# Kernel optimization log

Measured on AMD Instinct MI355X. Metric: run time of the kernel, lower is better.

Reference implementation:

```python
import jax, jax.numpy as jnp
import numpy as np

N, D, V = 4096, 512, 50000
K = 10  # accuracy_slack_size


def setup_inputs() -> dict:
    key = jax.random.key(0)
    k1, k2, k3, k4 = jax.random.split(key, 4)
    logits = jax.random.normal(k1, (N, D), dtype=jnp.float32)
    target = jax.random.randint(k2, (N,), 0, V, dtype=jnp.int64)
    mask = jax.random.randint(k3, (N,), 0, 2, dtype=jnp.int32)
    word_vectors = jax.random.normal(k4, (V, D), dtype=jnp.float32)
    return {"logits": logits, "target": target, "mask": mask, "word_vectors": word_vectors}


def reference(logits, target, mask, word_vectors):
    # Brute-force euclidean kNN: squared distances suffice for neighbor ranking.
    # d2[n, v] = ||x_n||^2 - 2 x_n . w_v + ||w_v||^2   -> [N, V]
    x2 = jnp.sum(logits * logits, axis=-1, keepdims=True)          # [N, 1]
    w2 = jnp.sum(word_vectors * word_vectors, axis=-1)             # [V]
    d2 = x2 - 2.0 * (logits @ word_vectors.T) + w2[None, :]        # [N, V]
    # top-K smallest distances -> indices of K nearest words
    _, words = jax.lax.top_k(-d2, K)                               # [N, K]
    # membership check: is the target word among the K neighbors
    hit = jnp.any(words == target[:, None], axis=-1)               # [N] bool
    m = mask.astype(jnp.float32)
    acc = jnp.sum(m * hit.astype(jnp.float32)) / jnp.sum(m)
    return jnp.reshape(acc, (1,))
```

## Files before the change

kernel.cpp:

```cpp
#include <hip/hip_runtime.h>
#include <stdint.h>

#define N_ROWS 4096
#define DIM    512
#define VOCAB  50000
#define VPAD   50048
#define TOPK   10
#define MARGIN 8.0f

typedef int i32x4 __attribute__((ext_vector_type(4)));

#define GLOBAL_AS __attribute__((address_space(1)))
#define LDS_AS    __attribute__((address_space(3)))

__device__ __forceinline__ void quant_row(const float* __restrict__ src,
                                          signed char* __restrict__ dst,
                                          int lane, float* rowmax_out,
                                          float* w2_out) {
    const float4* s4 = (const float4*)(src + lane * 8);
    float4 a = s4[0], b = s4[1];
    float mx = fmaxf(fmaxf(fmaxf(fabsf(a.x), fabsf(a.y)), fmaxf(fabsf(a.z), fabsf(a.w))),
                     fmaxf(fmaxf(fabsf(b.x), fabsf(b.y)), fmaxf(fabsf(b.z), fabsf(b.w))));
    float w2 = a.x*a.x + a.y*a.y + a.z*a.z + a.w*a.w
             + b.x*b.x + b.y*b.y + b.z*b.z + b.w*b.w;
    #pragma unroll
    for (int off = 1; off < 64; off <<= 1) {
        mx  = fmaxf(mx, __shfl_xor(mx, off, 64));
        w2 += __shfl_xor(w2, off, 64);
    }
    float inv = 127.0f / fmaxf(mx, 1e-30f);
    int q0 = (int)rintf(a.x * inv), q1 = (int)rintf(a.y * inv);
    int q2 = (int)rintf(a.z * inv), q3 = (int)rintf(a.w * inv);
    int q4 = (int)rintf(b.x * inv), q5 = (int)rintf(b.y * inv);
    int q6 = (int)rintf(b.z * inv), q7 = (int)rintf(b.w * inv);
    uint2 pk;
    pk.x = (q0 & 0xff) | ((q1 & 0xff) << 8) | ((q2 & 0xff) << 16) | ((unsigned)(q3 & 0xff) << 24);
    pk.y = (q4 & 0xff) | ((q5 & 0xff) << 8) | ((q6 & 0xff) << 16) | ((unsigned)(q7 & 0xff) << 24);
    *(uint2*)(dst + lane * 8) = pk;
    *rowmax_out = mx;
    *w2_out = w2;
}

#define PREP_Z  64
#define PREP_QX (PREP_Z + N_ROWS / 4)
#define PREP_QW (PREP_QX + VPAD / 4)
#define PREP_ST (PREP_QW + N_ROWS / 4)

__global__ __launch_bounds__(256) void prep_kernel(
        const float* __restrict__ X, const float* __restrict__ W,
        const int* __restrict__ target,
        signed char* __restrict__ Xq, signed char* __restrict__ Wq,
        float* __restrict__ sx, float* __restrict__ sw,
        float* __restrict__ w2, float* __restrict__ st,
        int* __restrict__ zbase) {
    const int b = blockIdx.x;
    const int wave = threadIdx.x >> 6, lane = threadIdx.x & 63;
    if (b < PREP_Z) {
        int i = b * 256 + threadIdx.x;
        if (i < 3 * N_ROWS + 16) zbase[i] = 0;
    } else if (b < PREP_QX) {
        int row = (b - PREP_Z) * 4 + wave;
        float mx, w2v;
        quant_row(X + (size_t)row * DIM, Xq + (size_t)row * DIM, lane, &mx, &w2v);
        if (lane == 0) sx[row] = fmaxf(mx, 1e-30f) / 127.0f;
    } else if (b < PREP_QW) {
        int row = (b - PREP_QX) * 4 + wave;
        if (row < VOCAB) {
            float mx, s2;
            quant_row(W + (size_t)row * DIM, Wq + (size_t)row * DIM, lane, &mx, &s2);
            if (lane == 0) { sw[row] = fmaxf(mx, 1e-30f) / 127.0f; w2[row] = s2; }
        } else {
            *(uint2*)(Wq + (size_t)row * DIM + lane * 8) = make_uint2(0, 0);
            if (lane == 0) { sw[row] = 0.0f; w2[row] = 1e30f; }
        }
    } else {
        int n = (b - PREP_QW) * 4 + wave;
        int t = target[n];
        const float4* x4 = (const float4*)(X + (size_t)n * DIM);
        const float4* w4 = (const float4*)(W + (size_t)t * DIM);
        float4 xa = x4[lane], xb = x4[lane + 64];
        float4 wa = w4[lane], wb = w4[lane + 64];
        float sxw = xa.x*wa.x + xa.y*wa.y + xa.z*wa.z + xa.w*wa.w
                  + xb.x*wb.x + xb.y*wb.y + xb.z*wb.z + xb.w*wb.w;
        float sww = wa.x*wa.x + wa.y*wa.y + wa.z*wa.z + wa.w*wa.w
                  + wb.x*wb.x + wb.y*wb.y + wb.z*wb.z + wb.w*wb.w;
        #pragma unroll
        for (int off = 32; off > 0; off >>= 1) {
            sxw += __shfl_down(sxw, off, 64);
            sww += __shfl_down(sww, off, 64);
        }
        if (lane == 0) st[n] = sww - 2.0f * sxw;
    }
}

__global__ __launch_bounds__(256) void count_mfma_i8(
        const signed char* __restrict__ Xq, const signed char* __restrict__ Wq,
        const float* __restrict__ sx, const float* __restrict__ sw,
        const float* __restrict__ w2, const float* __restrict__ st,
        const int* __restrict__ target,
        int* __restrict__ cnt_def, int* __restrict__ cnt_unc) {

    __shared__ signed char Als[128 * 64];
    __shared__ signed char Bls[128 * 64];
    __shared__ float w2_s[128];
    __shared__ float sw_s[128];
    __shared__ float st_s[128];
    __shared__ float sx_s[128];
    __shared__ int   t_s[128];
    __shared__ int   pk_s[128];

    const int tid  = threadIdx.x;
    const int wave = tid >> 6, lane = tid & 63;
    const int row0 = blockIdx.x * 128;
    const int col0 = blockIdx.y * 128;

    if (tid < 128) { w2_s[tid] = w2[col0 + tid]; sw_s[tid] = sw[col0 + tid]; pk_s[tid] = 0; }
    else           { st_s[tid - 128] = st[row0 + tid - 128];
                     sx_s[tid - 128] = sx[row0 + tid - 128];
                     t_s[tid - 128]  = target[row0 + tid - 128]; }

    const int ch = (lane & 3) ^ ((lane >> 3) & 3);
    const signed char* ga = Xq + (size_t)(row0 + wave*32 + (lane >> 2)) * DIM + ch * 16;
    const signed char* gb = Wq + (size_t)(col0 + wave*32 + (lane >> 2)) * DIM + ch * 16;
    signed char* la0 = &Als[(wave*32     ) * 64];
    signed char* la1 = &Als[(wave*32 + 16) * 64];
    signed char* lb0 = &Bls[(wave*32     ) * 64];
    signed char* lb1 = &Bls[(wave*32 + 16) * 64];

    const int q = lane >> 4, c = lane & 15;
    const int fs = (c >> 1) & 3;
    const int wm = wave >> 1, wn = wave & 1;
    const signed char* ap = &Als[(wm*64 + c) * 64 + (q ^ fs) * 16];
    const signed char* bp = &Bls[(wn*64 + c) * 64 + (q ^ fs) * 16];

    i32x4 acc[4][4];
    #pragma unroll
    for (int i = 0; i < 4; i++)
        #pragma unroll
        for (int j = 0; j < 4; j++) acc[i][j] = (i32x4){0, 0, 0, 0};

    for (int k0 = 0; k0 < DIM; k0 += 64) {
        __builtin_amdgcn_global_load_lds((const GLOBAL_AS void*)(ga + k0),           (LDS_AS void*)la0, 16, 0, 0);
        __builtin_amdgcn_global_load_lds((const GLOBAL_AS void*)(ga + 16*DIM + k0),  (LDS_AS void*)la1, 16, 0, 0);
        __builtin_amdgcn_global_load_lds((const GLOBAL_AS void*)(gb + k0),           (LDS_AS void*)lb0, 16, 0, 0);
        __builtin_amdgcn_global_load_lds((const GLOBAL_AS void*)(gb + 16*DIM + k0),  (LDS_AS void*)lb1, 16, 0, 0);
        __syncthreads();
        i32x4 af[4], bfr[4];
        #pragma unroll
        for (int i = 0; i < 4; i++) af[i]  = *(const i32x4*)(ap + i * 16 * 64);
        #pragma unroll
        for (int j = 0; j < 4; j++) bfr[j] = *(const i32x4*)(bp + j * 16 * 64);
        #pragma unroll
        for (int i = 0; i < 4; i++)
            #pragma unroll
            for (int j = 0; j < 4; j++)
                acc[i][j] = __builtin_amdgcn_mfma_i32_16x16x64_i8(af[i], bfr[j], acc[i][j], 0, 0, 0);
        __syncthreads();
    }

    #pragma unroll
    for (int i = 0; i < 4; i++) {
        #pragma unroll
        for (int reg = 0; reg < 4; reg++) {
            int r = wm*64 + i*16 + q*4 + reg;
            float stv = st_s[r];
            float sxr = sx_s[r];
            int   t   = t_s[r];
            int def = 0, unc = 0;
            #pragma unroll
            for (int j = 0; j < 4; j++) {
                int col_l = wn*64 + j*16 + c;
                float dot = sxr * sw_s[col_l] * (float)acc[i][j][reg];
                float s = w2_s[col_l] - 2.0f * dot;
                int v = col0 + col_l;
                if (v != t) {
                    if      (s < stv - MARGIN) def++;
                    else if (s < stv + MARGIN) unc++;
                }
            }
            int pk = (def << 16) | unc;
            pk += __shfl_xor(pk, 1, 64);
            pk += __shfl_xor(pk, 2, 64);
            pk += __shfl_xor(pk, 4, 64);
            pk += __shfl_xor(pk, 8, 64);
            if (c == 0) atomicAdd(&pk_s[r], pk);
        }
    }
    __syncthreads();
    if (tid < 128) {
        int pk = pk_s[tid];
        if (pk) {
            atomicAdd(&cnt_def[row0 + tid], pk >> 16);
            atomicAdd(&cnt_unc[row0 + tid], pk & 0xffff);
        }
    }
}

__global__ __launch_bounds__(256) void resolve3(const int* __restrict__ cnt_def,
                                                const int* __restrict__ cnt_unc,
                                                int* __restrict__ amb_rows,
                                                int* __restrict__ amb_count) {
    int n = blockIdx.x * 256 + threadIdx.x;
    if (n >= N_ROWS) return;
    int d = cnt_def[n], u = cnt_unc[n];
    if (d < TOPK && d + u >= TOPK) {
        int idx = atomicAdd(amb_count, 1);
        amb_rows[idx] = n;
    }
}

__device__ __forceinline__ int dot4i8(int a, int b, int acc) {
#if __has_builtin(__builtin_amdgcn_sdot4)
    return __builtin_amdgcn_sdot4(a, b, acc, false);
#else
    #pragma unroll
    for (int j = 0; j < 4; j++)
        acc += (int)(signed char)(a >> (8*j)) * (int)(signed char)(b >> (8*j));
    return acc;
#endif
}

__global__ __launch_bounds__(256) void band_scan(
        const signed char* __restrict__ Xq, const signed char* __restrict__ Wq,
        const float* __restrict__ X, const float* __restrict__ W,
        const float* __restrict__ sx, const float* __restrict__ sw,
        const float* __restrict__ w2, const float* __restrict__ st,
        const int* __restrict__ target,
        const int* __restrict__ amb_rows, const int* __restrict__ amb_count,
        int* __restrict__ count_exact) {
    const int lane = threadIdx.x & 63;
    const int wid  = (blockIdx.x << 2) | (threadIdx.x >> 6);
    const int nw   = gridDim.x << 2;
    const int namb = amb_count[0];
    for (int a = 0; a < namb; a++) {
        const int row = amb_rows[a];
        const int t   = target[row];
        const float sxr = sx[row], stv = st[row];
        const int2 xa8 = *(const int2*)(Xq + (size_t)row * DIM + lane * 8);
        for (int v = wid; v < VPAD; v += nw) {
            int2 wa8 = *(const int2*)(Wq + (size_t)v * DIM + lane * 8);
            int acc = dot4i8(xa8.x, wa8.x, 0);
            acc = dot4i8(xa8.y, wa8.y, acc);
            acc += __shfl_xor(acc, 1, 64);
            acc += __shfl_xor(acc, 2, 64);
            acc += __shfl_xor(acc, 4, 64);
            acc += __shfl_xor(acc, 8, 64);
            acc += __shfl_xor(acc, 16, 64);
            acc += __shfl_xor(acc, 32, 64);
            if (v == t) continue;
            float dot = sxr * sw[v] * (float)acc;
            float s = w2[v] - 2.0f * dot;
            if (!(s < stv - MARGIN) && (s < stv + MARGIN)) {
                const float4* xr = (const float4*)(X + (size_t)row * DIM + lane * 8);
                const float4* wr = (const float4*)(W + (size_t)v   * DIM + lane * 8);
                float4 x0 = xr[0], x1 = xr[1];
                float4 w0 = wr[0], w1 = wr[1];
                float p = x0.x*w0.x + x0.y*w0.y + x0.z*w0.z + x0.w*w0.w
                        + x1.x*w1.x + x1.y*w1.y + x1.z*w1.z + x1.w*w1.w;
                p += __shfl_xor(p, 1, 64);
                p += __shfl_xor(p, 2, 64);
                p += __shfl_xor(p, 4, 64);
                p += __shfl_xor(p, 8, 64);
                p += __shfl_xor(p, 16, 64);
                p += __shfl_xor(p, 32, 64);
                if (lane == 0) {
                    float se = w2[v] - 2.0f * p;
                    if (se < stv || (se == stv && v < t)) atomicAdd(&count_exact[row], 1);
                }
            }
        }
    }
}

__global__ __launch_bounds__(256) void finalize3(const int* __restrict__ cnt_def,
                                                 const int* __restrict__ cnt_unc,
                                                 const int* __restrict__ count_exact,
                                                 const int* __restrict__ mask,
                                                 float* __restrict__ out) {
    int tid = threadIdx.x;
    int hits = 0, msum = 0;
    for (int n = tid; n < N_ROWS; n += 256) {
        int m = mask[n];
        msum += m;
        int d = cnt_def[n], u = cnt_unc[n];
        int hv;
        if (d >= TOPK) hv = 0;
        else if (d + u < TOPK) hv = 1;
        else hv = (d + count_exact[n] < TOPK) ? 1 : 0;
        if (m) hits += hv;
    }
    #pragma unroll
    for (int off = 32; off > 0; off >>= 1) {
        hits += __shfl_down(hits, off, 64);
        msum += __shfl_down(msum, off, 64);
    }
    __shared__ int sh[8];
    int wid = tid >> 6, lane = tid & 63;
    if (lane == 0) { sh[wid] = hits; sh[4 + wid] = msum; }
    __syncthreads();
    if (tid == 0) {
        int H = sh[0] + sh[1] + sh[2] + sh[3];
        int M = sh[4] + sh[5] + sh[6] + sh[7];
        out[0] = (float)H / (float)M;
    }
}

#define BM 128
#define BN 128
#define BK 16
#define TM 8
#define TN 8

__global__ __launch_bounds__(64) void w2_kernel_fb(const float* __restrict__ W,
                                                   float* __restrict__ w2) {
    int v = blockIdx.x;
    const float4* w4 = (const float4*)(W + (size_t)v * DIM);
    int lane = threadIdx.x;
    float4 a = w4[lane];
    float4 b = w4[lane + 64];
    float s = a.x*a.x + a.y*a.y + a.z*a.z + a.w*a.w
            + b.x*b.x + b.y*b.y + b.z*b.z + b.w*b.w;
    #pragma unroll
    for (int off = 32; off > 0; off >>= 1) s += __shfl_down(s, off, 64);
    if (lane == 0) w2[v] = s;
}

__global__ __launch_bounds__(64) void st_kernel_fb(const float* __restrict__ X,
                                                   const float* __restrict__ W,
                                                   const int* __restrict__ target,
                                                   float* __restrict__ st) {
    int n = blockIdx.x;
    int t = target[n];
    const float4* x4 = (const float4*)(X + (size_t)n * DIM);
    const float4* w4 = (const float4*)(W + (size_t)t * DIM);
    int lane = threadIdx.x;
    float4 xa = x4[lane], xb = x4[lane + 64];
    float4 wa = w4[lane], wb = w4[lane + 64];
    float sxw = xa.x*wa.x + xa.y*wa.y + xa.z*wa.z + xa.w*wa.w
              + xb.x*wb.x + xb.y*wb.y + xb.z*wb.z + xb.w*wb.w;
    float sww = wa.x*wa.x + wa.y*wa.y + wa.z*wa.z + wa.w*wa.w
              + wb.x*wb.x + wb.y*wb.y + wb.z*wb.z + wb.w*wb.w;
    #pragma unroll
    for (int off = 32; off > 0; off >>= 1) {
        sxw += __shfl_down(sxw, off, 64);
        sww += __shfl_down(sww, off, 64);
    }
    if (lane == 0) st[n] = sww - 2.0f * sxw;
}

__global__ __launch_bounds__(256) void count_kernel_fb(
        const float* __restrict__ X, const float* __restrict__ W,
        const float* __restrict__ w2, const float* __restrict__ st,
        const int* __restrict__ target, int* __restrict__ count) {
    __shared__ float Xs[BK][BM];
    __shared__ float Ws[BK][BN];
    __shared__ float st_s[BM];
    __shared__ int   t_s[BM];
    __shared__ float w2_s[BN];
    const int tid  = threadIdx.x;
    const int row0 = blockIdx.y * BM;
    const int col0 = blockIdx.x * BN;
    if (tid < 128) { st_s[tid] = st[row0 + tid]; t_s[tid] = target[row0 + tid]; }
    else { int cc = tid - 128; int v = col0 + cc; if (v >= VOCAB) v = VOCAB - 1; w2_s[cc] = w2[v]; }
    float acc[TM][TN] = {};
    const int tx = tid & 15;
    const int ty = tid >> 4;
    for (int k0 = 0; k0 < DIM; k0 += BK) {
        #pragma unroll
        for (int j = 0; j < 2; j++) {
            int idx = tid + 256 * j;
            int r   = idx >> 2;
            int kq  = idx & 3;
            float4 xv = *(const float4*)(X + (size_t)(row0 + r) * DIM + k0 + kq * 4);
            Xs[kq*4+0][r] = xv.x; Xs[kq*4+1][r] = xv.y;
            Xs[kq*4+2][r] = xv.z; Xs[kq*4+3][r] = xv.w;
            int v = col0 + r; if (v >= VOCAB) v = VOCAB - 1;
            float4 wv = *(const float4*)(W + (size_t)v * DIM + k0 + kq * 4);
            Ws[kq*4+0][r] = wv.x; Ws[kq*4+1][r] = wv.y;
            Ws[kq*4+2][r] = wv.z; Ws[kq*4+3][r] = wv.w;
        }
        __syncthreads();
        #pragma unroll
        for (int kk = 0; kk < BK; kk++) {
            float a[TM], b[TN];
            #pragma unroll
            for (int i = 0; i < TM; i++) a[i] = Xs[kk][ty * TM + i];
            #pragma unroll
            for (int j = 0; j < TN; j++) b[j] = Ws[kk][tx * TN + j];
            #pragma unroll
            for (int i = 0; i < TM; i++)
                #pragma unroll
                for (int j = 0; j < TN; j++)
                    acc[i][j] += a[i] * b[j];
        }
        __syncthreads();
    }
    int cnt[TM];
    #pragma unroll
    for (int i = 0; i < TM; i++) {
        cnt[i] = 0;
        float stv = st_s[ty * TM + i];
        int   t   = t_s[ty * TM + i];
        #pragma unroll
        for (int j = 0; j < TN; j++) {
            int v = col0 + tx * TN + j;
            float s = w2_s[tx * TN + j] - 2.0f * acc[i][j];
            if (v < VOCAB && v != t && (s < stv || (s == stv && v < t))) cnt[i]++;
        }
    }
    __syncthreads();
    int* scnt = (int*)Xs;
    #pragma unroll
    for (int i = 0; i < TM; i++) scnt[(ty * TM + i) * 16 + tx] = cnt[i];
    __syncthreads();
    if (tid < BM) {
        int s = 0;
        #pragma unroll
        for (int j = 0; j < 16; j++) s += scnt[tid * 16 + j];
        atomicAdd(&count[row0 + tid], s);
    }
}

__global__ __launch_bounds__(256) void finalize_fb(const int* __restrict__ count,
                                                   const int* __restrict__ mask,
                                                   float* __restrict__ out) {
    int tid = threadIdx.x;
    int hits = 0, msum = 0;
    for (int n = tid; n < N_ROWS; n += 256) {
        int m = mask[n];
        msum += m;
        if (m && count[n] < TOPK) hits++;
    }
    #pragma unroll
    for (int off = 32; off > 0; off >>= 1) {
        hits += __shfl_down(hits, off, 64);
        msum += __shfl_down(msum, off, 64);
    }
    __shared__ int sh[8];
    int wid = tid >> 6, lane = tid & 63;
    if (lane == 0) { sh[wid] = hits; sh[4 + wid] = msum; }
    __syncthreads();
    if (tid == 0) {
        int H = sh[0] + sh[1] + sh[2] + sh[3];
        int M = sh[4] + sh[5] + sh[6] + sh[7];
        out[0] = (float)H / (float)M;
    }
}

extern "C" void kernel_launch(void* const* d_in, const int* in_sizes, int n_in,
                              void* d_out, int out_size, void* d_ws, size_t ws_size,
                              hipStream_t stream) {
    const float* X      = (const float*)d_in[0];
    const int*   target = (const int*)d_in[1];
    const int*   mask   = (const int*)d_in[2];
    const float* W      = (const float*)d_in[3];
    float* out = (float*)d_out;
    char* ws = (char*)d_ws;

    const size_t oXq  = 0;
    const size_t oWq  = oXq + (size_t)N_ROWS * DIM;
    const size_t osx  = oWq + (size_t)VPAD  * DIM;
    const size_t osw  = osx + (size_t)N_ROWS * 4;
    const size_t ow2  = osw + (size_t)VPAD * 4;
    const size_t ost  = ow2 + (size_t)VPAD * 4;
    const size_t ocd  = ost + (size_t)N_ROWS * 4;
    const size_t ocu  = ocd + (size_t)N_ROWS * 4;
    const size_t oce  = ocu + (size_t)N_ROWS * 4;
    const size_t octr = oce + (size_t)N_ROWS * 4;
    const size_t oamb = octr + 64;
    const size_t need = oamb + (size_t)N_ROWS * 4;

    if (ws_size >= need) {
        signed char* Xq = (signed char*)(ws + oXq);
        signed char* Wq = (signed char*)(ws + oWq);
        float* sx = (float*)(ws + osx);
        float* sw = (float*)(ws + osw);
        float* w2 = (float*)(ws + ow2);
        float* st = (float*)(ws + ost);
        int* cnt_def = (int*)(ws + ocd);
        int* cnt_unc = (int*)(ws + ocu);
        int* count_exact = (int*)(ws + oce);
        int* amb_count = (int*)(ws + octr);
        int* amb_rows = (int*)(ws + oamb);

        prep_kernel<<<PREP_ST, 256, 0, stream>>>(X, W, target, Xq, Wq, sx, sw, w2, st, cnt_def);
        count_mfma_i8<<<dim3(N_ROWS / 128, VPAD / 128), 256, 0, stream>>>(
            Xq, Wq, sx, sw, w2, st, target, cnt_def, cnt_unc);
        resolve3<<<16, 256, 0, stream>>>(cnt_def, cnt_unc, amb_rows, amb_count);
        band_scan<<<512, 256, 0, stream>>>(Xq, Wq, X, W, sx, sw, w2, st, target,
                                           amb_rows, amb_count, count_exact);
        finalize3<<<1, 256, 0, stream>>>(cnt_def, cnt_unc, count_exact, mask, out);
    } else {
        float* w2 = (float*)ws;
        float* st = (float*)(ws + 200704);
        int* countp = (int*)(ws + 200704 + 16384);
        hipMemsetAsync(countp, 0, N_ROWS * sizeof(int), stream);
        w2_kernel_fb<<<VOCAB, 64, 0, stream>>>(W, w2);
        st_kernel_fb<<<N_ROWS, 64, 0, stream>>>(X, W, target, st);
        dim3 grid((VOCAB + BN - 1) / BN, N_ROWS / BM);
        count_kernel_fb<<<grid, 256, 0, stream>>>(X, W, w2, st, target, countp);
        finalize_fb<<<1, 256, 0, stream>>>(countp, mask, out);
    }
}
```

Baseline: 416.4 us.

## Record per-tile uncertain counts and rescan only flagged tiles for ambiguous rows

The count kernel now writes a per-(vocab tile, row) byte recording how many uncertain candidates each 128-column tile produced. A new bandresolve kernel replaces resolve3 and band_scan. It checks for ambiguous rows on the fly, splits each row's tiles into four chunks across blocks, and rescans only the tiles flagged as uncertain instead of the whole vocabulary. This removes the full-vocabulary int8 rescan per ambiguous row and one kernel launch, at the cost of extra global writes (about 1.6 MB of flags) and a uint8 truncation of uncertain counts. The score is also computed with an fma.

```diff
diff --git a/kernel.cpp b/kernel.cpp
--- a/kernel.cpp
+++ b/kernel.cpp
@@ -5,6 +5,7 @@
 #define DIM    512
 #define VOCAB  50000
 #define VPAD   50048
+#define NTILES (VPAD / 128)
 #define TOPK   10
 #define MARGIN 8.0f
 
@@ -12,6 +13,12 @@
 
 #define GLOBAL_AS __attribute__((address_space(1)))
 #define LDS_AS    __attribute__((address_space(3)))
+
+__device__ __forceinline__ float s_score(float sxr, float swv, int acc, float w2v) {
+    float m  = sxr * swv;
+    float m2 = 2.0f * m;
+    return __builtin_fmaf(-m2, (float)acc, w2v);
+}
 
 __device__ __forceinline__ void quant_row(const float* __restrict__ src,
                                           signed char* __restrict__ dst,
@@ -57,7 +64,7 @@
     const int wave = threadIdx.x >> 6, lane = threadIdx.x & 63;
     if (b < PREP_Z) {
         int i = b * 256 + threadIdx.x;
-        if (i < 3 * N_ROWS + 16) zbase[i] = 0;
+        if (i < 3 * N_ROWS) zbase[i] = 0;
     } else if (b < PREP_QX) {
         int row = (b - PREP_Z) * 4 + wave;
         float mx, w2v;
@@ -98,7 +105,8 @@
         const float* __restrict__ sx, const float* __restrict__ sw,
         const float* __restrict__ w2, const float* __restrict__ st,
         const int* __restrict__ target,
-        int* __restrict__ cnt_def, int* __restrict__ cnt_unc) {
+        int* __restrict__ cnt_def, int* __restrict__ cnt_unc,
+        unsigned char* __restrict__ unc_tile) {
 
     __shared__ signed char Als[128 * 64];
     __shared__ signed char Bls[128 * 64];
@@ -165,17 +173,17 @@
             int r = wm*64 + i*16 + q*4 + reg;
             float stv = st_s[r];
             float sxr = sx_s[r];
+            float lo = stv - MARGIN, hi = stv + MARGIN;
             int   t   = t_s[r];
             int def = 0, unc = 0;
             #pragma unroll
             for (int j = 0; j < 4; j++) {
                 int col_l = wn*64 + j*16 + c;
-                float dot = sxr * sw_s[col_l] * (float)acc[i][j][reg];
-                float s = w2_s[col_l] - 2.0f * dot;
+                float s = s_score(sxr, sw_s[col_l], acc[i][j][reg], w2_s[col_l]);
                 int v = col0 + col_l;
                 if (v != t) {
-                    if      (s < stv - MARGIN) def++;
-                    else if (s < stv + MARGIN) unc++;
+                    if      (s < lo) def++;
+                    else if (s < hi) unc++;
                 }
             }
             int pk = (def << 16) | unc;
@@ -189,23 +197,11 @@
     __syncthreads();
     if (tid < 128) {
         int pk = pk_s[tid];
+        unc_tile[(size_t)blockIdx.y * N_ROWS + row0 + tid] = (unsigned char)(pk & 0xffff);
         if (pk) {
             atomicAdd(&cnt_def[row0 + tid], pk >> 16);
             atomicAdd(&cnt_unc[row0 + tid], pk & 0xffff);
         }
-    }
-}
-
-__global__ __launch_bounds__(256) void resolve3(const int* __restrict__ cnt_def,
-                                                const int* __restrict__ cnt_unc,
-                                                int* __restrict__ amb_rows,
-                                                int* __restrict__ amb_count) {
-    int n = blockIdx.x * 256 + threadIdx.x;
-    if (n >= N_ROWS) return;
-    int d = cnt_def[n], u = cnt_unc[n];
-    if (d < TOPK && d + u >= TOPK) {
-        int idx = atomicAdd(amb_count, 1);
-        amb_rows[idx] = n;
     }
 }
 
@@ -220,52 +216,58 @@
 #endif
 }
 
-__global__ __launch_bounds__(256) void band_scan(
+__global__ __launch_bounds__(256) void bandresolve(
         const signed char* __restrict__ Xq, const signed char* __restrict__ Wq,
         const float* __restrict__ X, const float* __restrict__ W,
         const float* __restrict__ sx, const float* __restrict__ sw,
         const float* __restrict__ w2, const float* __restrict__ st,
         const int* __restrict__ target,
-        const int* __restrict__ amb_rows, const int* __restrict__ amb_count,
+        const int* __restrict__ cnt_def, const int* __restrict__ cnt_unc,
+        const unsigned char* __restrict__ unc_tile,
         int* __restrict__ count_exact) {
-    const int lane = threadIdx.x & 63;
-    const int wid  = (blockIdx.x << 2) | (threadIdx.x >> 6);
-    const int nw   = gridDim.x << 2;
-    const int namb = amb_count[0];
-    for (int a = 0; a < namb; a++) {
-        const int row = amb_rows[a];
-        const int t   = target[row];
+    const int wave = threadIdx.x >> 6, lane = threadIdx.x & 63;
+    for (int u = blockIdx.x; u < N_ROWS * 4; u += gridDim.x) {
+        const int row = u >> 2, qt = u & 3;
+        const int d = cnt_def[row], un = cnt_unc[row];
+        if (d >= TOPK || d + un < TOPK) continue;
+        const int t = target[row];
         const float sxr = sx[row], stv = st[row];
+        const float lo = stv - MARGIN, hi = stv + MARGIN;
         const int2 xa8 = *(const int2*)(Xq + (size_t)row * DIM + lane * 8);
-        for (int v = wid; v < VPAD; v += nw) {
-            int2 wa8 = *(const int2*)(Wq + (size_t)v * DIM + lane * 8);
-            int acc = dot4i8(xa8.x, wa8.x, 0);
-            acc = dot4i8(xa8.y, wa8.y, acc);
-            acc += __shfl_xor(acc, 1, 64);
-            acc += __shfl_xor(acc, 2, 64);
-            acc += __shfl_xor(acc, 4, 64);
-            acc += __shfl_xor(acc, 8, 64);
-            acc += __shfl_xor(acc, 16, 64);
-            acc += __shfl_xor(acc, 32, 64);
-            if (v == t) continue;
-            float dot = sxr * sw[v] * (float)acc;
-            float s = w2[v] - 2.0f * dot;
-            if (!(s < stv - MARGIN) && (s < stv + MARGIN)) {
-                const float4* xr = (const float4*)(X + (size_t)row * DIM + lane * 8);
-                const float4* wr = (const float4*)(W + (size_t)v   * DIM + lane * 8);
-                float4 x0 = xr[0], x1 = xr[1];
-                float4 w0 = wr[0], w1 = wr[1];
-                float p = x0.x*w0.x + x0.y*w0.y + x0.z*w0.z + x0.w*w0.w
-                        + x1.x*w1.x + x1.y*w1.y + x1.z*w1.z + x1.w*w1.w;
-                p += __shfl_xor(p, 1, 64);
-                p += __shfl_xor(p, 2, 64);
-                p += __shfl_xor(p, 4, 64);
-                p += __shfl_xor(p, 8, 64);
-                p += __shfl_xor(p, 16, 64);
-                p += __shfl_xor(p, 32, 64);
-                if (lane == 0) {
-                    float se = w2[v] - 2.0f * p;
-                    if (se < stv || (se == stv && v < t)) atomicAdd(&count_exact[row], 1);
+        const int t0 = qt * 98;
+        const int t1 = (t0 + 98 < NTILES) ? t0 + 98 : NTILES;
+        for (int tl = t0; tl < t1; tl++) {
+            if (unc_tile[(size_t)tl * N_ROWS + row] == 0) continue;
+            for (int wi = wave; wi < 128; wi += 4) {
+                int v = tl * 128 + wi;
+                if (v == t) continue;
+                int2 wa8 = *(const int2*)(Wq + (size_t)v * DIM + lane * 8);
+                int acc = dot4i8(xa8.x, wa8.x, 0);
+                acc = dot4i8(xa8.y, wa8.y, acc);
+                acc += __shfl_xor(acc, 1, 64);
+                acc += __shfl_xor(acc, 2, 64);
+                acc += __shfl_xor(acc, 4, 64);
+                acc += __shfl_xor(acc, 8, 64);
+                acc += __shfl_xor(acc, 16, 64);
+                acc += __shfl_xor(acc, 32, 64);
+                float s = s_score(sxr, sw[v], acc, w2[v]);
+                if (!(s < lo) && (s < hi)) {
+                    const float4* xr = (const float4*)(X + (size_t)row * DIM + lane * 8);
+                    const float4* wr = (const float4*)(W + (size_t)v   * DIM + lane * 8);
+                    float4 x0 = xr[0], x1 = xr[1];
+                    float4 w0 = wr[0], w1 = wr[1];
+                    float p = x0.x*w0.x + x0.y*w0.y + x0.z*w0.z + x0.w*w0.w
+                            + x1.x*w1.x + x1.y*w1.y + x1.z*w1.z + x1.w*w1.w;
+                    p += __shfl_xor(p, 1, 64);
+                    p += __shfl_xor(p, 2, 64);
+                    p += __shfl_xor(p, 4, 64);
+                    p += __shfl_xor(p, 8, 64);
+                    p += __shfl_xor(p, 16, 64);
+                    p += __shfl_xor(p, 32, 64);
+                    if (lane == 0) {
+                        float se = w2[v] - 2.0f * p;
+                        if (se < stv || (se == stv && v < t)) atomicAdd(&count_exact[row], 1);
+                    }
                 }
             }
         }
@@ -466,9 +468,8 @@
     const size_t ocd  = ost + (size_t)N_ROWS * 4;
     const size_t ocu  = ocd + (size_t)N_ROWS * 4;
     const size_t oce  = ocu + (size_t)N_ROWS * 4;
-    const size_t octr = oce + (size_t)N_ROWS * 4;
-    const size_t oamb = octr + 64;
-    const size_t need = oamb + (size_t)N_ROWS * 4;
+    const size_t oflg = oce + (size_t)N_ROWS * 4;
+    const size_t need = oflg + (size_t)NTILES * N_ROWS;
 
     if (ws_size >= need) {
         signed char* Xq = (signed char*)(ws + oXq);
@@ -480,15 +481,13 @@
         int* cnt_def = (int*)(ws + ocd);
         int* cnt_unc = (int*)(ws + ocu);
         int* count_exact = (int*)(ws + oce);
-        int* amb_count = (int*)(ws + octr);
-        int* amb_rows = (int*)(ws + oamb);
+        unsigned char* unc_tile = (unsigned char*)(ws + oflg);
 
         prep_kernel<<<PREP_ST, 256, 0, stream>>>(X, W, target, Xq, Wq, sx, sw, w2, st, cnt_def);
         count_mfma_i8<<<dim3(N_ROWS / 128, VPAD / 128), 256, 0, stream>>>(
-            Xq, Wq, sx, sw, w2, st, target, cnt_def, cnt_unc);
-        resolve3<<<16, 256, 0, stream>>>(cnt_def, cnt_unc, amb_rows, amb_count);
-        band_scan<<<512, 256, 0, stream>>>(Xq, Wq, X, W, sx, sw, w2, st, target,
-                                           amb_rows, amb_count, count_exact);
+            Xq, Wq, sx, sw, w2, st, target, cnt_def, cnt_unc, unc_tile);
+        bandresolve<<<1024, 256, 0, stream>>>(Xq, Wq, X, W, sx, sw, w2, st, target,
+                                              cnt_def, cnt_unc, unc_tile, count_exact);
         finalize3<<<1, 256, 0, stream>>>(cnt_def, cnt_unc, count_exact, mask, out);
     } else {
         float* w2 = (float*)ws;
```

After: 517.2 us. 24.2% more time.

## Give each wave private LDS tiles to drop block barriers in the K loop

Applied to the files above, without the earlier changes.

Each of the four waves now stages its own 64-row A and 64-row B slices into a private LDS region. It synchronises with s_waitcnt on vmcnt and lgkmcnt instead of two __syncthreads per K step, and a single barrier is kept before the epilogue. The aim is to remove block-wide barrier stalls in the int8 MFMA GEMM loop. In exchange, every A and B slice is now fetched by two waves, which doubles global and L2 traffic and LDS footprint. The loop is also still not double-buffered, so load latency remains exposed per wave.

```diff
diff --git a/kernel.cpp b/kernel.cpp
--- a/kernel.cpp
+++ b/kernel.cpp
@@ -100,8 +100,8 @@
         const int* __restrict__ target,
         int* __restrict__ cnt_def, int* __restrict__ cnt_unc) {
 
-    __shared__ signed char Als[128 * 64];
-    __shared__ signed char Bls[128 * 64];
+    __shared__ signed char Als[4][64 * 64];
+    __shared__ signed char Bls[4][64 * 64];
     __shared__ float w2_s[128];
     __shared__ float sw_s[128];
     __shared__ float st_s[128];
@@ -119,19 +119,17 @@
                      sx_s[tid - 128] = sx[row0 + tid - 128];
                      t_s[tid - 128]  = target[row0 + tid - 128]; }
 
+    const int wm = wave >> 1, wn = wave & 1;
     const int ch = (lane & 3) ^ ((lane >> 3) & 3);
-    const signed char* ga = Xq + (size_t)(row0 + wave*32 + (lane >> 2)) * DIM + ch * 16;
-    const signed char* gb = Wq + (size_t)(col0 + wave*32 + (lane >> 2)) * DIM + ch * 16;
-    signed char* la0 = &Als[(wave*32     ) * 64];
-    signed char* la1 = &Als[(wave*32 + 16) * 64];
-    signed char* lb0 = &Bls[(wave*32     ) * 64];
-    signed char* lb1 = &Bls[(wave*32 + 16) * 64];
+    const signed char* ga = Xq + (size_t)(row0 + wm*64 + (lane >> 2)) * DIM + ch * 16;
+    const signed char* gb = Wq + (size_t)(col0 + wn*64 + (lane >> 2)) * DIM + ch * 16;
+    signed char* la = Als[wave];
+    signed char* lb = Bls[wave];
 
     const int q = lane >> 4, c = lane & 15;
     const int fs = (c >> 1) & 3;
-    const int wm = wave >> 1, wn = wave & 1;
-    const signed char* ap = &Als[(wm*64 + c) * 64 + (q ^ fs) * 16];
-    const signed char* bp = &Bls[(wn*64 + c) * 64 + (q ^ fs) * 16];
+    const signed char* ap = &la[c * 64 + (q ^ fs) * 16];
+    const signed char* bp = &lb[c * 64 + (q ^ fs) * 16];
 
     i32x4 acc[4][4];
     #pragma unroll
@@ -140,11 +138,15 @@
         for (int j = 0; j < 4; j++) acc[i][j] = (i32x4){0, 0, 0, 0};
 
     for (int k0 = 0; k0 < DIM; k0 += 64) {
-        __builtin_amdgcn_global_load_lds((const GLOBAL_AS void*)(ga + k0),           (LDS_AS void*)la0, 16, 0, 0);
-        __builtin_amdgcn_global_load_lds((const GLOBAL_AS void*)(ga + 16*DIM + k0),  (LDS_AS void*)la1, 16, 0, 0);
-        __builtin_amdgcn_global_load_lds((const GLOBAL_AS void*)(gb + k0),           (LDS_AS void*)lb0, 16, 0, 0);
-        __builtin_amdgcn_global_load_lds((const GLOBAL_AS void*)(gb + 16*DIM + k0),  (LDS_AS void*)lb1, 16, 0, 0);
-        __syncthreads();
+        __asm__ volatile("s_waitcnt lgkmcnt(0)" ::: "memory");
+        #pragma unroll
+        for (int g = 0; g < 4; g++) {
+            __builtin_amdgcn_global_load_lds((const GLOBAL_AS void*)(ga + (size_t)(g*16)*DIM + k0),
+                                             (LDS_AS void*)(la + g*16*64), 16, 0, 0);
+            __builtin_amdgcn_global_load_lds((const GLOBAL_AS void*)(gb + (size_t)(g*16)*DIM + k0),
+                                             (LDS_AS void*)(lb + g*16*64), 16, 0, 0);
+        }
+        __asm__ volatile("s_waitcnt vmcnt(0)" ::: "memory");
         i32x4 af[4], bfr[4];
         #pragma unroll
         for (int i = 0; i < 4; i++) af[i]  = *(const i32x4*)(ap + i * 16 * 64);
@@ -155,8 +157,9 @@
             #pragma unroll
             for (int j = 0; j < 4; j++)
                 acc[i][j] = __builtin_amdgcn_mfma_i32_16x16x64_i8(af[i], bfr[j], acc[i][j], 0, 0, 0);
-        __syncthreads();
-    }
+    }
+
+    __syncthreads();
 
     #pragma unroll
     for (int i = 0; i < 4; i++) {
```

Result: slower. 439.9 us (+5.6%).
